# Kernel tuning notes

Hardware: AMD Instinct MI355X
Metric: run time of the kernel (lower is better)

Reference implementation:

```python
import jax, jax.numpy as jnp
import numpy as np

EPS = 1e-7  # K.epsilon()
NUM_CAPSULE = 32
DIM_CAPSULE = 16
ROUTINGS = 3


def squash(x, axis=-1):
    # NOTE: this repo's squash is pure L2 normalization (no |s|^2/(1+|s|^2) factor)
    s2 = jnp.sum(jnp.square(x), axis=axis, keepdims=True)
    return x / jnp.sqrt(s2 + EPS)


def setup_inputs() -> dict:
    key = jax.random.key(0)
    k1, k2 = jax.random.split(key)
    B, L, D_IN = 32, 2048, 64
    u_vecs = jax.random.normal(k1, (B, L, D_IN), dtype=jnp.float32)
    # glorot-ish scale for the capsule kernel
    W = jax.random.normal(k2, (1, D_IN, NUM_CAPSULE * DIM_CAPSULE), dtype=jnp.float32) * 0.05
    return {"u_vecs": u_vecs, "W": W}


def reference(u_vecs, W):
    B, L, _ = u_vecs.shape
    # K.conv1d with kernel size 1 == pointwise matmul
    u_hat = jnp.einsum('bli,io->blo', u_vecs, W[0])
    u_hat = u_hat.reshape(B, L, NUM_CAPSULE, DIM_CAPSULE)
    u_hat = jnp.transpose(u_hat, (0, 2, 1, 3))  # [B, nc, L, dc]

    b = jnp.zeros((B, NUM_CAPSULE, L), dtype=u_hat.dtype)
    outputs = None
    for i in range(ROUTINGS):
        # softmax over the num_capsule axis (axis=1), per the permute dance in the source
        c = jax.nn.softmax(b, axis=1)  # [B, nc, L]
        outputs = squash(jnp.einsum('bnl,bnld->bnd', c, u_hat))  # [B, nc, dc]
        if i < ROUTINGS - 1:
            b = jnp.einsum('bnd,bnld->bnl', outputs, u_hat)  # overwrite, not accumulate
    return outputs
```

## Files before the change

kernel.cpp:

```cpp
#include <hip/hip_runtime.h>

#define NC 32
#define DC 16
#define LSEQ 2048

__global__ __launch_bounds__(256) void k_sum_u(const float* __restrict__ u,
                                               float* __restrict__ v0p) {
    int b  = blockIdx.x >> 3;
    int l0 = (blockIdx.x & 7) * 256;
    int q  = threadIdx.x & 15;
    int r  = threadIdx.x >> 4;
    const float4* u4 = (const float4*)u;
    float4 acc = {0.f, 0.f, 0.f, 0.f};
#pragma unroll
    for (int j = 0; j < 16; ++j) {
        int l = l0 + r + 16 * j;
        float4 x = u4[(b * LSEQ + l) * 16 + q];
        acc.x += x.x; acc.y += x.y; acc.z += x.z; acc.w += x.w;
    }
    __shared__ float red[16][64];
    red[r][q * 4 + 0] = acc.x;
    red[r][q * 4 + 1] = acc.y;
    red[r][q * 4 + 2] = acc.z;
    red[r][q * 4 + 3] = acc.w;
    __syncthreads();
    if (threadIdx.x < 64) {
        float s = 0.f;
#pragma unroll
        for (int rr = 0; rr < 16; ++rr) s += red[rr][threadIdx.x];
        v0p[blockIdx.x * 64 + threadIdx.x] = s;
    }
}

template <bool BCAST, bool FINAL>
__global__ __launch_bounds__(64) void k_caps(const float* __restrict__ v,
                                             const float* __restrict__ W,
                                             float* __restrict__ wtil,
                                             float* __restrict__ out,
                                             float vscale) {
    int b  = blockIdx.x >> 3;
    int ng = blockIdx.x & 7;
    int t  = threadIdx.x;
    __shared__ float vS[4][72];
    __shared__ float oS[4][16];
    if (BCAST) {
        float s = 0.f;
#pragma unroll
        for (int ch = 0; ch < 8; ++ch) s += v[(b * 8 + ch) * 64 + t];
        s *= vscale;
#pragma unroll
        for (int n4 = 0; n4 < 4; ++n4) vS[n4][t] = s;
    } else {
        int row = t >> 4, col4 = t & 15;
        const float4* v4 = (const float4*)v;
        float4 a = {0.f, 0.f, 0.f, 0.f};
#pragma unroll
        for (int ch = 0; ch < 16; ++ch) {
            float4 x = v4[(b * 16 + ch) * 512 + (ng * 4 + row) * 16 + col4];
            a.x += x.x; a.y += x.y; a.z += x.z; a.w += x.w;
        }
        ((float4*)&vS[row][0])[col4] = a;
    }
    __syncthreads();
    int n4 = t >> 4, d = t & 15;
    int n  = ng * 4 + n4;
    const float* vrow = &vS[n4][0];
    float s = 0.f;
#pragma unroll
    for (int i = 0; i < 64; ++i)
        s = fmaf(vrow[i], W[i * (NC * DC) + n * DC + d], s);
    float s2 = s * s;
#pragma unroll
    for (int off = 8; off >= 1; off >>= 1) s2 += __shfl_xor(s2, off, 16);
    float o = s / sqrtf(s2 + 1e-7f);
    if (FINAL) {
        out[b * (NC * DC) + n * DC + d] = o;
    } else {
        oS[n4][d] = o;
        __syncthreads();
        int i4 = t & 15;
        float4 wv;
        float* wvp = (float*)&wv;
#pragma unroll
        for (int k = 0; k < 4; ++k) {
            int i = i4 * 4 + k;
            float acc = 0.f;
#pragma unroll
            for (int dd = 0; dd < 16; ++dd)
                acc = fmaf(W[i * (NC * DC) + n * DC + dd], oS[n4][dd], acc);
            wvp[k] = acc;
        }
        ((float4*)wtil)[(b * (NC * 64) + n * 64 + i4 * 4) >> 2] = wv;
    }
}

__global__ __launch_bounds__(256) void k_route(const float* __restrict__ u,
                                               const float* __restrict__ wtil,
                                               float* __restrict__ vpart) {
    int b    = blockIdx.x >> 4;
    int ch   = blockIdx.x & 15;
    int l0   = ch * 128;
    int t    = threadIdx.x;
    int w    = t >> 6;
    int lane = t & 63;
    int lr   = lane & 7;
    int lc   = lane >> 3;
    int dr   = lane & 7;
    int ng   = lane >> 3;

    __shared__ float uS[128 * 68];
    __shared__ float wS[32 * 68];
    __shared__ float cS[128 * 36];
    float4* uS4 = (float4*)uS;
    float4* wS4 = (float4*)wS;
    float4* c4  = (float4*)cS;

    const float4* ug = (const float4*)(u + (b * LSEQ + l0) * 64);
#pragma unroll
    for (int r = 0; r < 8; ++r) {
        int idx = t + 256 * r;
        uS4[(idx >> 4) * 17 + (idx & 15)] = ug[idx];
    }
    const float4* wg = (const float4*)(wtil + b * (NC * 64));
#pragma unroll
    for (int r = 0; r < 2; ++r) {
        int idx = t + 256 * r;
        wS4[(idx >> 4) * 17 + (idx & 15)] = wg[idx];
    }
    __syncthreads();

    float acc[4][4];
#pragma unroll
    for (int i = 0; i < 4; ++i)
#pragma unroll
        for (int jj = 0; jj < 4; ++jj) acc[i][jj] = 0.f;
    int arow = w * 32 + lr;
#pragma unroll 4
    for (int k4 = 0; k4 < 16; ++k4) {
        float4 wf[4];
#pragma unroll
        for (int jj = 0; jj < 4; ++jj) wf[jj] = wS4[(lc + 8 * jj) * 17 + k4];
#pragma unroll
        for (int i = 0; i < 4; ++i) {
            float4 a = uS4[(arow + 8 * i) * 17 + k4];
#pragma unroll
            for (int jj = 0; jj < 4; ++jj) {
                acc[i][jj] = fmaf(a.x, wf[jj].x, acc[i][jj]);
                acc[i][jj] = fmaf(a.y, wf[jj].y, acc[i][jj]);
                acc[i][jj] = fmaf(a.z, wf[jj].z, acc[i][jj]);
                acc[i][jj] = fmaf(a.w, wf[jj].w, acc[i][jj]);
            }
        }
    }

#pragma unroll
    for (int i = 0; i < 4; ++i) {
        float m = fmaxf(fmaxf(acc[i][0], acc[i][1]), fmaxf(acc[i][2], acc[i][3]));
        m = fmaxf(m, __shfl_xor(m, 8));
        m = fmaxf(m, __shfl_xor(m, 16));
        m = fmaxf(m, __shfl_xor(m, 32));
        float e0 = __expf(acc[i][0] - m), e1 = __expf(acc[i][1] - m);
        float e2 = __expf(acc[i][2] - m), e3 = __expf(acc[i][3] - m);
        float ss = e0 + e1 + e2 + e3;
        ss += __shfl_xor(ss, 8);
        ss += __shfl_xor(ss, 16);
        ss += __shfl_xor(ss, 32);
        float inv = 1.f / ss;
        float4 cvv = {e0 * inv, e1 * inv, e2 * inv, e3 * inv};
        c4[(arow + 8 * i) * 9 + lc] = cvv;
    }
    __syncthreads();

    float vacc[4][8];
#pragma unroll
    for (int jj = 0; jj < 4; ++jj)
#pragma unroll
        for (int k = 0; k < 8; ++k) vacc[jj][k] = 0.f;
#pragma unroll 8
    for (int lrel = 0; lrel < 32; ++lrel) {
        int row = w * 32 + lrel;
        float4 cv = c4[row * 9 + ng];
        const float4* ur = uS4 + row * 17 + dr * 2;
        float4 u0 = ur[0], u1 = ur[1];
        float* cp = (float*)&cv;
#pragma unroll
        for (int jj = 0; jj < 4; ++jj) {
            float c = cp[jj];
            vacc[jj][0] = fmaf(c, u0.x, vacc[jj][0]);
            vacc[jj][1] = fmaf(c, u0.y, vacc[jj][1]);
            vacc[jj][2] = fmaf(c, u0.z, vacc[jj][2]);
            vacc[jj][3] = fmaf(c, u0.w, vacc[jj][3]);
            vacc[jj][4] = fmaf(c, u1.x, vacc[jj][4]);
            vacc[jj][5] = fmaf(c, u1.y, vacc[jj][5]);
            vacc[jj][6] = fmaf(c, u1.z, vacc[jj][6]);
            vacc[jj][7] = fmaf(c, u1.w, vacc[jj][7]);
        }
    }
    __syncthreads();

    float* red   = uS;
    float* rbase = red + (w >> 1) * 2048;
    if (w & 1) {
#pragma unroll
        for (int jj = 0; jj < 4; ++jj) {
            float4* rp = (float4*)(rbase + (ng + 8 * jj) * 64 + dr * 8);
            float4 r0 = {vacc[jj][0], vacc[jj][1], vacc[jj][2], vacc[jj][3]};
            float4 r1 = {vacc[jj][4], vacc[jj][5], vacc[jj][6], vacc[jj][7]};
            rp[0] = r0;
            rp[1] = r1;
        }
    }
    __syncthreads();
    if (!(w & 1)) {
#pragma unroll
        for (int jj = 0; jj < 4; ++jj) {
            float4* rp = (float4*)(rbase + (ng + 8 * jj) * 64 + dr * 8);
            float4 r0 = rp[0], r1 = rp[1];
            r0.x += vacc[jj][0]; r0.y += vacc[jj][1];
            r0.z += vacc[jj][2]; r0.w += vacc[jj][3];
            r1.x += vacc[jj][4]; r1.y += vacc[jj][5];
            r1.z += vacc[jj][6]; r1.w += vacc[jj][7];
            rp[0] = r0;
            rp[1] = r1;
        }
    }
    __syncthreads();
    float4* red4 = (float4*)red;
    float4* vp4  = (float4*)(vpart + blockIdx.x * 2048);
#pragma unroll
    for (int s = 0; s < 2; ++s) {
        int idx4 = t + 256 * s;
        float4 a  = red4[idx4];
        float4 c2 = red4[512 + idx4];
        float4 o  = {a.x + c2.x, a.y + c2.y, a.z + c2.z, a.w + c2.w};
        vp4[idx4] = o;
    }
}

extern "C" void kernel_launch(void* const* d_in, const int* in_sizes, int n_in,
                              void* d_out, int out_size, void* d_ws, size_t ws_size,
                              hipStream_t stream) {
    const float* u = (const float*)d_in[0];
    const float* W = (const float*)d_in[1];
    float* out = (float*)d_out;
    float* ws  = (float*)d_ws;
    float* v0p   = ws;
    float* wt    = ws + 16384;
    float* vpart = ws + 16384 + 65536;

    k_sum_u<<<256, 256, 0, stream>>>(u, v0p);
    k_caps<true, false><<<256, 64, 0, stream>>>(v0p, W, wt, nullptr, 1.0f / 32.0f);
    k_route<<<512, 256, 0, stream>>>(u, wt, vpart);
    k_caps<false, false><<<256, 64, 0, stream>>>(vpart, W, wt, nullptr, 1.0f);
    k_route<<<512, 256, 0, stream>>>(u, wt, vpart);
    k_caps<false, true><<<256, 64, 0, stream>>>(vpart, W, nullptr, out, 1.0f);
}
```

Measured before the change: 100.0 us.

## Fuse capsule squash and W-projection into routing kernel, drop intermediate launches

Removes the separate k_caps kernels between routing passes. Each k_route block now reduces the partial capsule sums, computes the squashed outputs and the projected W~ tile itself. This saves two kernel launches and the wtil round trip through global memory. In exchange, every one of the 16 blocks per batch redundantly recomputes the same 64x512 projection and re-reads W, and vpart is double-buffered.

```diff
diff --git a/kernel.cpp b/kernel.cpp
--- a/kernel.cpp
+++ b/kernel.cpp
@@ -32,25 +32,14 @@
     }
 }
 
-template <bool BCAST, bool FINAL>
-__global__ __launch_bounds__(64) void k_caps(const float* __restrict__ v,
-                                             const float* __restrict__ W,
-                                             float* __restrict__ wtil,
-                                             float* __restrict__ out,
-                                             float vscale) {
+__global__ __launch_bounds__(64) void k_caps_final(const float* __restrict__ v,
+                                                   const float* __restrict__ W,
+                                                   float* __restrict__ out) {
     int b  = blockIdx.x >> 3;
     int ng = blockIdx.x & 7;
     int t  = threadIdx.x;
     __shared__ float vS[4][72];
-    __shared__ float oS[4][16];
-    if (BCAST) {
-        float s = 0.f;
-#pragma unroll
-        for (int ch = 0; ch < 8; ++ch) s += v[(b * 8 + ch) * 64 + t];
-        s *= vscale;
-#pragma unroll
-        for (int n4 = 0; n4 < 4; ++n4) vS[n4][t] = s;
-    } else {
+    {
         int row = t >> 4, col4 = t & 15;
         const float4* v4 = (const float4*)v;
         float4 a = {0.f, 0.f, 0.f, 0.f};
@@ -72,30 +61,13 @@
     float s2 = s * s;
 #pragma unroll
     for (int off = 8; off >= 1; off >>= 1) s2 += __shfl_xor(s2, off, 16);
-    float o = s / sqrtf(s2 + 1e-7f);
-    if (FINAL) {
-        out[b * (NC * DC) + n * DC + d] = o;
-    } else {
-        oS[n4][d] = o;
-        __syncthreads();
-        int i4 = t & 15;
-        float4 wv;
-        float* wvp = (float*)&wv;
-#pragma unroll
-        for (int k = 0; k < 4; ++k) {
-            int i = i4 * 4 + k;
-            float acc = 0.f;
-#pragma unroll
-            for (int dd = 0; dd < 16; ++dd)
-                acc = fmaf(W[i * (NC * DC) + n * DC + dd], oS[n4][dd], acc);
-            wvp[k] = acc;
-        }
-        ((float4*)wtil)[(b * (NC * 64) + n * 64 + i4 * 4) >> 2] = wv;
-    }
-}
-
+    out[b * (NC * DC) + n * DC + d] = s / sqrtf(s2 + 1e-7f);
+}
+
+template <int ITER0>
 __global__ __launch_bounds__(256) void k_route(const float* __restrict__ u,
-                                               const float* __restrict__ wtil,
+                                               const float* __restrict__ W,
+                                               const float* __restrict__ vin,
                                                float* __restrict__ vpart) {
     int b    = blockIdx.x >> 4;
     int ch   = blockIdx.x & 15;
@@ -111,6 +83,7 @@
     __shared__ float uS[128 * 68];
     __shared__ float wS[32 * 68];
     __shared__ float cS[128 * 36];
+    __shared__ float oS[512];
     float4* uS4 = (float4*)uS;
     float4* wS4 = (float4*)wS;
     float4* c4  = (float4*)cS;
@@ -121,11 +94,68 @@
         int idx = t + 256 * r;
         uS4[(idx >> 4) * 17 + (idx & 15)] = ug[idx];
     }
-    const float4* wg = (const float4*)(wtil + b * (NC * 64));
-#pragma unroll
-    for (int r = 0; r < 2; ++r) {
-        int idx = t + 256 * r;
-        wS4[(idx >> 4) * 17 + (idx & 15)] = wg[idx];
+
+    float* vS = cS;
+    if (ITER0) {
+        if (t < 64) {
+            float s = 0.f;
+#pragma unroll
+            for (int c = 0; c < 8; ++c) s += vin[(b * 8 + c) * 64 + t];
+            vS[t] = s * (1.f / 32.f);
+        }
+    } else {
+        const float4* vp = (const float4*)(vin + b * 16 * 2048);
+#pragma unroll
+        for (int r = 0; r < 2; ++r) {
+            int idx = t + 256 * r;
+            float4 s = {0.f, 0.f, 0.f, 0.f};
+#pragma unroll
+            for (int c = 0; c < 16; ++c) {
+                float4 x = vp[c * 512 + idx];
+                s.x += x.x; s.y += x.y; s.z += x.z; s.w += x.w;
+            }
+            ((float4*)vS)[(idx >> 4) * 17 + (idx & 15)] = s;
+        }
+    }
+    __syncthreads();
+
+#pragma unroll
+    for (int rep = 0; rep < 2; ++rep) {
+        int nd = t + 256 * rep;
+        const float* vrow = ITER0 ? vS : vS + (nd >> 4) * 68;
+        float s = 0.f;
+#pragma unroll 8
+        for (int i = 0; i < 64; ++i)
+            s = fmaf(vrow[i], W[i * (NC * DC) + nd], s);
+        float s2 = s * s;
+        s2 += __shfl_xor(s2, 1);
+        s2 += __shfl_xor(s2, 2);
+        s2 += __shfl_xor(s2, 4);
+        s2 += __shfl_xor(s2, 8);
+        oS[nd] = s / sqrtf(s2 + 1e-7f);
+    }
+    __syncthreads();
+
+#pragma unroll
+    for (int rep = 0; rep < 2; ++rep) {
+        int f4 = t + 256 * rep;
+        int n = f4 >> 4, i4 = f4 & 15;
+        const float4* o4 = (const float4*)(oS + n * DC);
+        float4 ov0 = o4[0], ov1 = o4[1], ov2 = o4[2], ov3 = o4[3];
+        float4 wv;
+        float* wvp = (float*)&wv;
+#pragma unroll
+        for (int k = 0; k < 4; ++k) {
+            int i = i4 * 4 + k;
+            const float4* wr = (const float4*)(W + i * (NC * DC) + n * DC);
+            float4 w0 = wr[0], w1 = wr[1], w2 = wr[2], w3 = wr[3];
+            float acc = w0.x * ov0.x + w0.y * ov0.y + w0.z * ov0.z + w0.w * ov0.w;
+            acc += w1.x * ov1.x + w1.y * ov1.y + w1.z * ov1.z + w1.w * ov1.w;
+            acc += w2.x * ov2.x + w2.y * ov2.y + w2.z * ov2.z + w2.w * ov2.w;
+            acc += w3.x * ov3.x + w3.y * ov3.y + w3.z * ov3.z + w3.w * ov3.w;
+            wvp[k] = acc;
+        }
+        wS4[n * 17 + i4] = wv;
     }
     __syncthreads();
 
@@ -244,14 +274,12 @@
     const float* W = (const float*)d_in[1];
     float* out = (float*)d_out;
     float* ws  = (float*)d_ws;
-    float* v0p   = ws;
-    float* wt    = ws + 16384;
-    float* vpart = ws + 16384 + 65536;
+    float* v0p = ws;
+    float* vpA = ws + 16384;
+    float* vpB = ws + 16384 + 1048576;
 
     k_sum_u<<<256, 256, 0, stream>>>(u, v0p);
-    k_caps<true, false><<<256, 64, 0, stream>>>(v0p, W, wt, nullptr, 1.0f / 32.0f);
-    k_route<<<512, 256, 0, stream>>>(u, wt, vpart);
-    k_caps<false, false><<<256, 64, 0, stream>>>(vpart, W, wt, nullptr, 1.0f);
-    k_route<<<512, 256, 0, stream>>>(u, wt, vpart);
-    k_caps<false, true><<<256, 64, 0, stream>>>(vpart, W, nullptr, out, 1.0f);
-}
+    k_route<1><<<512, 256, 0, stream>>>(u, W, v0p, vpA);
+    k_route<0><<<512, 256, 0, stream>>>(u, W, vpA, vpB);
+    k_caps_final<<<256, 64, 0, stream>>>(vpB, W, out);
+}
```

Result: slower. 119.5 us (+19.5%).

## Store u and wtil as fp16 in LDS, use fdot2, halve route tile

Applied to the files above, without the earlier changes.

The routing kernel now converts u and the routing weights to packed fp16 in shared memory. It computes the logits with v_dot2 fp32-accumulate instructions, and unpacks to fp32 for the weighted sum. Each block covers 64 rows instead of 128, so the grid grows to 1024 blocks. Shared memory shrinks, which allows more resident blocks per CU, and k_caps now reduces 32 partials instead of 16. The change risks accuracy from fp16 rounding of the inputs and adds conversion overhead plus a larger partial-sum reduction.

```diff
diff --git a/kernel.cpp b/kernel.cpp
--- a/kernel.cpp
+++ b/kernel.cpp
@@ -3,6 +3,18 @@
 #define NC 32
 #define DC 16
 #define LSEQ 2048
+
+typedef __fp16 h2 __attribute__((ext_vector_type(2)));
+union F4H { float4 f; h2 h[4]; };
+union H2F2 { h2 h[2]; float2 f; };
+
+__device__ __forceinline__ float fdot2f(h2 a, h2 b, float c) {
+#if __has_builtin(__builtin_amdgcn_fdot2)
+    return __builtin_amdgcn_fdot2(a, b, c, false);
+#else
+    return c + (float)a[0] * (float)b[0] + (float)a[1] * (float)b[1];
+#endif
+}
 
 __global__ __launch_bounds__(256) void k_sum_u(const float* __restrict__ u,
                                                float* __restrict__ v0p) {
@@ -55,8 +67,8 @@
         const float4* v4 = (const float4*)v;
         float4 a = {0.f, 0.f, 0.f, 0.f};
 #pragma unroll
-        for (int ch = 0; ch < 16; ++ch) {
-            float4 x = v4[(b * 16 + ch) * 512 + (ng * 4 + row) * 16 + col4];
+        for (int ch = 0; ch < 32; ++ch) {
+            float4 x = v4[(b * 32 + ch) * 512 + (ng * 4 + row) * 16 + col4];
             a.x += x.x; a.y += x.y; a.z += x.z; a.w += x.w;
         }
         ((float4*)&vS[row][0])[col4] = a;
@@ -94,12 +106,12 @@
     }
 }
 
-__global__ __launch_bounds__(256) void k_route(const float* __restrict__ u,
-                                               const float* __restrict__ wtil,
-                                               float* __restrict__ vpart) {
-    int b    = blockIdx.x >> 4;
-    int ch   = blockIdx.x & 15;
-    int l0   = ch * 128;
+__global__ __launch_bounds__(256, 4) void k_route(const float* __restrict__ u,
+                                                  const float* __restrict__ wtil,
+                                                  float* __restrict__ vpart) {
+    int b    = blockIdx.x >> 5;
+    int ch   = blockIdx.x & 31;
+    int l0   = ch * 64;
     int t    = threadIdx.x;
     int w    = t >> 6;
     int lane = t & 63;
@@ -108,53 +120,64 @@
     int dr   = lane & 7;
     int ng   = lane >> 3;
 
-    __shared__ float uS[128 * 68];
-    __shared__ float wS[32 * 68];
-    __shared__ float cS[128 * 36];
-    float4* uS4 = (float4*)uS;
-    float4* wS4 = (float4*)wS;
-    float4* c4  = (float4*)cS;
+    __shared__ float smem[5760];
+    float* uA2f = smem;
+    float* wS2f = smem + 2304;
+    float* cS   = smem + 3456;
+    const float4* uA2_4 = (const float4*)uA2f;
+    const float4* wS2_4 = (const float4*)wS2f;
+    float4* c4 = (float4*)cS;
 
     const float4* ug = (const float4*)(u + (b * LSEQ + l0) * 64);
 #pragma unroll
-    for (int r = 0; r < 8; ++r) {
+    for (int r = 0; r < 4; ++r) {
         int idx = t + 256 * r;
-        uS4[(idx >> 4) * 17 + (idx & 15)] = ug[idx];
-    }
-    const float4* wg = (const float4*)(wtil + b * (NC * 64));
-#pragma unroll
-    for (int r = 0; r < 2; ++r) {
-        int idx = t + 256 * r;
-        wS4[(idx >> 4) * 17 + (idx & 15)] = wg[idx];
-    }
-    __syncthreads();
-
-    float acc[4][4];
-#pragma unroll
-    for (int i = 0; i < 4; ++i)
+        float4 x = ug[idx];
+        H2F2 p;
+        p.h[0][0] = (__fp16)x.x; p.h[0][1] = (__fp16)x.y;
+        p.h[1][0] = (__fp16)x.z; p.h[1][1] = (__fp16)x.w;
+        *(float2*)(uA2f + (idx >> 4) * 36 + (idx & 15) * 2) = p.f;
+    }
+    {
+        const float4* wg = (const float4*)(wtil + b * (NC * 64));
+#pragma unroll
+        for (int r = 0; r < 2; ++r) {
+            int idx = t + 256 * r;
+            float4 x = wg[idx];
+            H2F2 p;
+            p.h[0][0] = (__fp16)x.x; p.h[0][1] = (__fp16)x.y;
+            p.h[1][0] = (__fp16)x.z; p.h[1][1] = (__fp16)x.w;
+            *(float2*)(wS2f + (idx >> 4) * 36 + (idx & 15) * 2) = p.f;
+        }
+    }
+    __syncthreads();
+
+    float acc[2][4];
+#pragma unroll
+    for (int i = 0; i < 2; ++i)
 #pragma unroll
         for (int jj = 0; jj < 4; ++jj) acc[i][jj] = 0.f;
-    int arow = w * 32 + lr;
-#pragma unroll 4
-    for (int k4 = 0; k4 < 16; ++k4) {
-        float4 wf[4];
-#pragma unroll
-        for (int jj = 0; jj < 4; ++jj) wf[jj] = wS4[(lc + 8 * jj) * 17 + k4];
-#pragma unroll
-        for (int i = 0; i < 4; ++i) {
-            float4 a = uS4[(arow + 8 * i) * 17 + k4];
+    int arow = w * 16 + lr;
+#pragma unroll
+    for (int k8 = 0; k8 < 8; ++k8) {
+        F4H wf[4];
+#pragma unroll
+        for (int jj = 0; jj < 4; ++jj) wf[jj].f = wS2_4[(lc + 8 * jj) * 9 + k8];
+#pragma unroll
+        for (int i = 0; i < 2; ++i) {
+            F4H av;
+            av.f = uA2_4[(arow + 8 * i) * 9 + k8];
 #pragma unroll
             for (int jj = 0; jj < 4; ++jj) {
-                acc[i][jj] = fmaf(a.x, wf[jj].x, acc[i][jj]);
-                acc[i][jj] = fmaf(a.y, wf[jj].y, acc[i][jj]);
-                acc[i][jj] = fmaf(a.z, wf[jj].z, acc[i][jj]);
-                acc[i][jj] = fmaf(a.w, wf[jj].w, acc[i][jj]);
+#pragma unroll
+                for (int m = 0; m < 4; ++m)
+                    acc[i][jj] = fdot2f(av.h[m], wf[jj].h[m], acc[i][jj]);
             }
         }
     }
 
 #pragma unroll
-    for (int i = 0; i < 4; ++i) {
+    for (int i = 0; i < 2; ++i) {
         float m = fmaxf(fmaxf(acc[i][0], acc[i][1]), fmaxf(acc[i][2], acc[i][3]));
         m = fmaxf(m, __shfl_xor(m, 8));
         m = fmaxf(m, __shfl_xor(m, 16));
@@ -177,28 +200,29 @@
 #pragma unroll
         for (int k = 0; k < 8; ++k) vacc[jj][k] = 0.f;
 #pragma unroll 8
-    for (int lrel = 0; lrel < 32; ++lrel) {
-        int row = w * 32 + lrel;
+    for (int lrel = 0; lrel < 16; ++lrel) {
+        int row = w * 16 + lrel;
         float4 cv = c4[row * 9 + ng];
-        const float4* ur = uS4 + row * 17 + dr * 2;
-        float4 u0 = ur[0], u1 = ur[1];
+        F4H uu;
+        uu.f = *(const float4*)(uA2f + row * 36 + dr * 4);
+        float uf[8];
+#pragma unroll
+        for (int k = 0; k < 4; ++k) {
+            uf[2 * k + 0] = (float)uu.h[k][0];
+            uf[2 * k + 1] = (float)uu.h[k][1];
+        }
         float* cp = (float*)&cv;
 #pragma unroll
         for (int jj = 0; jj < 4; ++jj) {
             float c = cp[jj];
-            vacc[jj][0] = fmaf(c, u0.x, vacc[jj][0]);
-            vacc[jj][1] = fmaf(c, u0.y, vacc[jj][1]);
-            vacc[jj][2] = fmaf(c, u0.z, vacc[jj][2]);
-            vacc[jj][3] = fmaf(c, u0.w, vacc[jj][3]);
-            vacc[jj][4] = fmaf(c, u1.x, vacc[jj][4]);
-            vacc[jj][5] = fmaf(c, u1.y, vacc[jj][5]);
-            vacc[jj][6] = fmaf(c, u1.z, vacc[jj][6]);
-            vacc[jj][7] = fmaf(c, u1.w, vacc[jj][7]);
-        }
-    }
-    __syncthreads();
-
-    float* red   = uS;
+#pragma unroll
+            for (int k = 0; k < 8; ++k)
+                vacc[jj][k] = fmaf(c, uf[k], vacc[jj][k]);
+        }
+    }
+    __syncthreads();
+
+    float* red   = smem;
     float* rbase = red + (w >> 1) * 2048;
     if (w & 1) {
 #pragma unroll
@@ -250,8 +274,8 @@
 
     k_sum_u<<<256, 256, 0, stream>>>(u, v0p);
     k_caps<true, false><<<256, 64, 0, stream>>>(v0p, W, wt, nullptr, 1.0f / 32.0f);
-    k_route<<<512, 256, 0, stream>>>(u, wt, vpart);
+    k_route<<<1024, 256, 0, stream>>>(u, wt, vpart);
     k_caps<false, false><<<256, 64, 0, stream>>>(vpart, W, wt, nullptr, 1.0f);
-    k_route<<<512, 256, 0, stream>>>(u, wt, vpart);
+    k_route<<<1024, 256, 0, stream>>>(u, wt, vpart);
     k_caps<false, true><<<256, 64, 0, stream>>>(vpart, W, nullptr, out, 1.0f);
 }
```

After: 102.0 us. About the same (+1.9%).
